# Performance work log

Hardware: AMD Instinct MI355X
Metric: run time of the kernel (lower is better)

The kernel has to match this reference:

```python
import jax, jax.numpy as jnp
import numpy as np

N = 50000      # nodes
E = 800000     # edges (before self-loops)
F_IN = 256
H = 8          # heads layer 1
C = 64         # hidden channels per head
OUT = 40       # classes
NEG_SLOPE = 0.2


def setup_inputs() -> dict:
    key = jax.random.key(0)
    ks = jax.random.split(key, 10)
    sc = 0.05
    return {
        "x": jax.random.normal(ks[0], (N, F_IN), jnp.float32),
        "edge_index": jax.random.randint(ks[1], (2, E), 0, N, dtype=jnp.int64),
        "W1": jax.random.normal(ks[2], (F_IN, H * C), jnp.float32) * sc,
        "a_src1": jax.random.normal(ks[3], (H, C), jnp.float32) * sc,
        "a_dst1": jax.random.normal(ks[4], (H, C), jnp.float32) * sc,
        "b1": jnp.zeros((H * C,), jnp.float32),
        "W2": jax.random.normal(ks[5], (H * C, OUT), jnp.float32) * sc,
        "a_src2": jax.random.normal(ks[6], (1, OUT), jnp.float32) * sc,
        "a_dst2": jax.random.normal(ks[7], (1, OUT), jnp.float32) * sc,
        "b2": jnp.zeros((OUT,), jnp.float32),
    }


def gat_layer(h_in, src, dst, W, a_s, a_d, b, heads, ch, concat, n):
    # h: [n, heads, ch] per-head linear transform
    h = (h_in @ W).reshape(n, heads, ch)
    alpha_s = jnp.sum(h * a_s, axis=-1)   # [n, heads]
    alpha_d = jnp.sum(h * a_d, axis=-1)   # [n, heads]
    # edge-wise raw attention logits [E, heads]
    e = jax.nn.leaky_relu(alpha_s[src] + alpha_d[dst], NEG_SLOPE)
    # segment softmax over incoming edges of each dst node
    m = jax.ops.segment_max(e, dst, num_segments=n)
    w = jnp.exp(e - m[dst])
    s = jax.ops.segment_sum(w, dst, num_segments=n)
    alpha = w / s[dst]                    # [E, heads]
    # scatter-aggregate messages: [n, heads, ch]
    out = jax.ops.segment_sum(h[src] * alpha[:, :, None], dst, num_segments=n)
    out = out.reshape(n, heads * ch) if concat else out.mean(axis=1)
    return out + b


def reference(x, edge_index, W1, a_src1, a_dst1, b1, W2, a_src2, a_dst2, b2):
    # add self-loops (PyG GATConv default); guarantees every dst has >=1 edge
    loop = jnp.arange(N, dtype=edge_index.dtype)
    src = jnp.concatenate([edge_index[0], loop])
    dst = jnp.concatenate([edge_index[1], loop])
    h = gat_layer(x, src, dst, W1, a_src1, a_dst1, b1, H, C, True, N)
    h = jax.nn.relu(h)  # dropout is identity in eval mode
    out = gat_layer(h, src, dst, W2, a_src2, a_dst2, b2, 1, OUT, False, N)
    return jax.nn.log_softmax(out, axis=1)
```

## Files before the change

### kernel.cpp

```cpp
#include <hip/hip_runtime.h>

#define N_NODES 50000
#define N_EDGES 800000
#define F_INK   256
#define HC      512
#define OUT_C   40
#define OUT_P   48
#define NEG     0.2f
#define CAP     64
#define GEMM_NB 782
#define CHUNKS  782
#define PART_SZ 6250
#define SCAT_NB (CHUNKS * 8)

typedef short short8 __attribute__((ext_vector_type(8)));
typedef float f32x4 __attribute__((ext_vector_type(4)));
typedef float f32x2 __attribute__((ext_vector_type(2)));

__device__ __forceinline__ float bf2f(unsigned short u) {
    union { unsigned int i; float f; } v; v.i = ((unsigned int)u) << 16; return v.f;
}
__device__ __forceinline__ unsigned short f2bf(float f) {
    union { float f; unsigned int i; } v; v.f = f;
    unsigned int x = v.i;
    return (unsigned short)((x + 0x7fffu + ((x >> 16) & 1u)) >> 16);
}
__device__ __forceinline__ float bflo(unsigned int u) {
    union { unsigned int i; float f; } v; v.i = u << 16; return v.f;
}
__device__ __forceinline__ float bfhi(unsigned int u) {
    union { unsigned int i; float f; } v; v.i = u & 0xffff0000u; return v.f;
}
__device__ __forceinline__ bool ei_is64(const int* ei) {
    return ei[1] == 0 && ei[3] == 0 && ei[5] == 0;
}
__device__ __forceinline__ float lrelu(float x) { return fmaxf(x, NEG * x); }
__device__ __forceinline__ unsigned char f2fp8(float v) {
    return (unsigned char)(__builtin_amdgcn_cvt_pk_fp8_f32(v, v, 0, false) & 0xff);
}
__device__ __forceinline__ float fp82f(unsigned char b) {
    f32x2 p = __builtin_amdgcn_cvt_pk_f32_fp8((int)b, false);
    return p[0];
}

__global__ __launch_bounds__(256) void prep_k(const float* __restrict__ W1, const float* __restrict__ W2,
                       const float* __restrict__ s1, const float* __restrict__ d1, const float* __restrict__ b1,
                       const float* __restrict__ s2, const float* __restrict__ d2, const float* __restrict__ b2,
                       unsigned short* __restrict__ W1p, unsigned short* __restrict__ W2p,
                       unsigned short* __restrict__ s1c, unsigned short* __restrict__ d1c,
                       unsigned short* __restrict__ b1c, unsigned short* __restrict__ s2c,
                       unsigned short* __restrict__ d2c, unsigned short* __restrict__ b2c,
                       int* __restrict__ cnt) {
    int b = blockIdx.x;
    if (b < 512) {
        int t = b * 256 + threadIdx.x;
        int k = t / HC, n = t % HC;
        int s = k >> 5, q = (k >> 3) & 3, j = k & 7;
        W1p[((((s << 2) + q) * HC + n) << 3) + j] = f2bf(W1[k * HC + n]);
    } else if (b < 608) {
        int t = (b - 512) * 256 + threadIdx.x;
        int k = t / OUT_P, n = t % OUT_P;
        int s = k >> 5, q = (k >> 3) & 3, j = k & 7;
        unsigned short v = (n < OUT_C) ? f2bf(W2[k * OUT_C + n]) : (unsigned short)0;
        W2p[((((s << 2) + q) * OUT_P + n) << 3) + j] = v;
    } else if (b == 608) {
        int t = threadIdx.x;
        for (int j = t; j < 512; j += 256) {
            s1c[j] = f2bf(s1[j]); d1c[j] = f2bf(d1[j]); b1c[j] = f2bf(b1[j]);
        }
        if (t < OUT_C) { s2c[t] = f2bf(s2[t]); d2c[t] = f2bf(d2[t]); b2c[t] = f2bf(b2[t]); }
    } else {
        int i = (b - 609) * 256 + threadIdx.x;
        if (i < N_NODES) cnt[i * 16] = 0;
    }
}

__global__ __launch_bounds__(256) void scat_k(const int* __restrict__ ei,
                                              int* __restrict__ cnt, int* __restrict__ srcs) {
    int tid = threadIdx.x;
    int part = blockIdx.x & 7;
    int chunk = blockIdx.x >> 3;
    int lo = part * PART_SZ;
    bool is64 = ei_is64(ei);
    int e0 = chunk * 1024 + (tid << 2);
    int s[4], d[4];
    bool vld[4];
    if (chunk < CHUNKS - 1) {
        if (is64) {
            int4 a0 = *reinterpret_cast<const int4*>(ei + 2 * e0);
            int4 a1 = *reinterpret_cast<const int4*>(ei + 2 * e0 + 4);
            int4 c0 = *reinterpret_cast<const int4*>(ei + 2 * N_EDGES + 2 * e0);
            int4 c1 = *reinterpret_cast<const int4*>(ei + 2 * N_EDGES + 2 * e0 + 4);
            s[0] = a0.x; s[1] = a0.z; s[2] = a1.x; s[3] = a1.z;
            d[0] = c0.x; d[1] = c0.z; d[2] = c1.x; d[3] = c1.z;
        } else {
            int4 a0 = *reinterpret_cast<const int4*>(ei + e0);
            int4 c0 = *reinterpret_cast<const int4*>(ei + N_EDGES + e0);
            s[0] = a0.x; s[1] = a0.y; s[2] = a0.z; s[3] = a0.w;
            d[0] = c0.x; d[1] = c0.y; d[2] = c0.z; d[3] = c0.w;
        }
        vld[0] = vld[1] = vld[2] = vld[3] = true;
    } else {
#pragma unroll
        for (int j = 0; j < 4; j++) {
            int e = e0 + j;
            vld[j] = e < N_EDGES;
            int ec = vld[j] ? e : 0;
            s[j] = is64 ? ei[2 * ec] : ei[ec];
            d[j] = is64 ? ei[2 * N_EDGES + 2 * ec] : ei[N_EDGES + ec];
        }
    }
#pragma unroll
    for (int j = 0; j < 4; j++) {
        int dj = d[j];
        if (vld[j] && dj >= lo && dj < lo + PART_SZ) {
            int pos = atomicAdd(&cnt[dj * 16], 1);
            if (pos < CAP) srcs[(size_t)dj * CAP + pos] = s[j];
        }
    }
}

__global__ __launch_bounds__(256) void gemm1_k(const float* __restrict__ x,
                                               const unsigned short* __restrict__ Wp,
                                               const unsigned short* __restrict__ a_s,
                                               const unsigned short* __restrict__ a_d,
                                               unsigned char* __restrict__ h1f8,
                                               float* __restrict__ as1, float* __restrict__ ad1) {
    __shared__ unsigned short xs[64 * 264];
    int tid = threadIdx.x;
    int bm = blockIdx.x;
    int row0 = bm * 64;
#pragma unroll
    for (int it = 0; it < 16; it++) {
        int j = tid + it * 256;
        int r = j >> 6;
        int c = (j & 63) << 2;
        int rr = row0 + r; rr = rr < N_NODES ? rr : N_NODES - 1;
        float4 f = *reinterpret_cast<const float4*>(x + (size_t)rr * F_INK + c);
        unsigned int lo = (unsigned int)f2bf(f.x) | ((unsigned int)f2bf(f.y) << 16);
        unsigned int hi = (unsigned int)f2bf(f.z) | ((unsigned int)f2bf(f.w) << 16);
        *reinterpret_cast<uint2*>(&xs[r * 264 + c]) = make_uint2(lo, hi);
    }
    __syncthreads();
    int w = tid >> 6, lane = tid & 63;
    int q = lane >> 4, l16 = lane & 15;
    short8 a[8];
#pragma unroll
    for (int s = 0; s < 8; s++)
        a[s] = *reinterpret_cast<const short8*>(&xs[(w * 16 + l16) * 264 + s * 32 + q * 8]);
    int orow = row0 + w * 16 + q * 4;
#pragma unroll
    for (int bn = 0; bn < 8; bn++) {
        f32x4 acc[4];
#pragma unroll
        for (int t = 0; t < 4; t++) acc[t] = (f32x4){0.f, 0.f, 0.f, 0.f};
#pragma unroll
        for (int s = 0; s < 8; s++) {
#pragma unroll
            for (int t = 0; t < 4; t++) {
                int col = bn * 64 + t * 16 + l16;
                short8 b = *reinterpret_cast<const short8*>(Wp + ((((s << 2) + q) * HC + col) << 3));
                acc[t] = __builtin_amdgcn_mfma_f32_16x16x32_bf16(a[s], b, acc[t], 0, 0, 0);
            }
        }
        float sa0 = 0.f, sa1 = 0.f, sa2 = 0.f, sa3 = 0.f;
        float da0 = 0.f, da1 = 0.f, da2 = 0.f, da3 = 0.f;
#pragma unroll
        for (int t = 0; t < 4; t++) {
            int col = bn * 64 + t * 16 + l16;
            float asc = bf2f(a_s[col]);
            float adc = bf2f(a_d[col]);
            float v0 = acc[t][0], v1 = acc[t][1], v2 = acc[t][2], v3 = acc[t][3];
            sa0 += v0 * asc; da0 += v0 * adc;
            sa1 += v1 * asc; da1 += v1 * adc;
            sa2 += v2 * asc; da2 += v2 * adc;
            sa3 += v3 * asc; da3 += v3 * adc;
            if (orow + 3 < N_NODES) {
                h1f8[(size_t)(orow + 0) * HC + col] = f2fp8(v0);
                h1f8[(size_t)(orow + 1) * HC + col] = f2fp8(v1);
                h1f8[(size_t)(orow + 2) * HC + col] = f2fp8(v2);
                h1f8[(size_t)(orow + 3) * HC + col] = f2fp8(v3);
            } else {
                if (orow + 0 < N_NODES) h1f8[(size_t)(orow + 0) * HC + col] = f2fp8(v0);
                if (orow + 1 < N_NODES) h1f8[(size_t)(orow + 1) * HC + col] = f2fp8(v1);
                if (orow + 2 < N_NODES) h1f8[(size_t)(orow + 2) * HC + col] = f2fp8(v2);
                if (orow + 3 < N_NODES) h1f8[(size_t)(orow + 3) * HC + col] = f2fp8(v3);
            }
        }
#pragma unroll
        for (int m = 1; m < 16; m <<= 1) {
            sa0 += __shfl_xor(sa0, m, 64); sa1 += __shfl_xor(sa1, m, 64);
            sa2 += __shfl_xor(sa2, m, 64); sa3 += __shfl_xor(sa3, m, 64);
            da0 += __shfl_xor(da0, m, 64); da1 += __shfl_xor(da1, m, 64);
            da2 += __shfl_xor(da2, m, 64); da3 += __shfl_xor(da3, m, 64);
        }
        if (l16 < 4) {
            int rr = orow + l16;
            float sav = (l16 == 0) ? sa0 : (l16 == 1) ? sa1 : (l16 == 2) ? sa2 : sa3;
            float dav = (l16 == 0) ? da0 : (l16 == 1) ? da1 : (l16 == 2) ? da2 : da3;
            if (rr < N_NODES) { as1[rr * 8 + bn] = sav; ad1[rr * 8 + bn] = dav; }
        }
    }
}

#define ACC16(u, wgt)                                                              \
    {                                                                              \
        f32x2 q0 = __builtin_amdgcn_cvt_pk_f32_fp8((int)(u).x, false);             \
        f32x2 q1 = __builtin_amdgcn_cvt_pk_f32_fp8((int)(u).x, true);              \
        f32x2 q2 = __builtin_amdgcn_cvt_pk_f32_fp8((int)(u).y, false);             \
        f32x2 q3 = __builtin_amdgcn_cvt_pk_f32_fp8((int)(u).y, true);              \
        f32x2 q4 = __builtin_amdgcn_cvt_pk_f32_fp8((int)(u).z, false);             \
        f32x2 q5 = __builtin_amdgcn_cvt_pk_f32_fp8((int)(u).z, true);              \
        f32x2 q6 = __builtin_amdgcn_cvt_pk_f32_fp8((int)(u).w, false);             \
        f32x2 q7 = __builtin_amdgcn_cvt_pk_f32_fp8((int)(u).w, true);              \
        f32x2 wv = {(wgt), (wgt)};                                                 \
        ac[0] += wv * q0; ac[1] += wv * q1; ac[2] += wv * q2; ac[3] += wv * q3;    \
        ac[4] += wv * q4; ac[5] += wv * q5; ac[6] += wv * q6; ac[7] += wv * q7;    \
    }

__global__ __launch_bounds__(256) void agg1_k(const unsigned char* __restrict__ h1f8,
                                              const float* __restrict__ as1,
                                              const float* __restrict__ ad1,
                                              const int* __restrict__ cnt,
                                              const int* __restrict__ srcs,
                                              const unsigned short* __restrict__ b1,
                                              const unsigned short* __restrict__ W2p,
                                              const unsigned short* __restrict__ a_s2,
                                              const unsigned short* __restrict__ a_d2,
                                              unsigned char* __restrict__ h2f8) {
    __shared__ unsigned short rows[16 * 520];
    __shared__ int sSrc[16 * CAP];
    __shared__ int sCnt[16];
    __shared__ float sAs[16], sAd[16];
    __shared__ int ctr;
    int tid = threadIdx.x;
    int base = blockIdx.x * 16;
    reinterpret_cast<int4*>(sSrc)[tid] =
        reinterpret_cast<const int4*>(srcs + (size_t)base * CAP)[tid];
    if (tid < 16) {
        int d = cnt[(base + tid) * 16];
        sCnt[tid] = d < CAP ? d : CAP;
        sAs[tid] = 0.f; sAd[tid] = 0.f;
    }
    if (tid == 0) ctr = 0;
    __syncthreads();
    int w = tid >> 6, lane = tid & 63;
    int half = lane >> 5, li = lane & 31;
    int h = li >> 2;
    uint4 ub0 = reinterpret_cast<const uint4*>(b1)[li * 2 + 0];
    uint4 ub1 = reinterpret_cast<const uint4*>(b1)[li * 2 + 1];
    for (;;) {
        int rl = 0;
        if (lane == 0) rl = atomicAdd(&ctr, 1);
        rl = __shfl(rl, 0, 64);
        if (rl >= 16) break;
        int wid = base + rl;
        float adv = ad1[wid * 8 + h];
        const int* sp = sSrc + rl * CAP;
        int deg = sCnt[rl];
        f32x2 ac[8];
#pragma unroll
        for (int k = 0; k < 8; k++) ac[k] = (f32x2){0.f, 0.f};
        float sumw = 0.f;
        {
            int s = half ? (deg > 0 ? sp[0] : wid) : wid;
            float A = as1[s * 8 + h];
            uint4 u = reinterpret_cast<const uint4*>(h1f8 + (size_t)s * HC)[li];
            float wj = (half && deg == 0) ? 0.f : __expf(lrelu(A + adv));
            sumw += wj;
            ACC16(u, wj)
        }
        int v = 1;
        for (; v + 16 <= deg; v += 16) {
            int s[8]; float A[8]; uint4 u[8];
#pragma unroll
            for (int j = 0; j < 8; j++) s[j] = sp[v + 2 * j + half];
#pragma unroll
            for (int j = 0; j < 8; j++) A[j] = as1[s[j] * 8 + h];
#pragma unroll
            for (int j = 0; j < 8; j++)
                u[j] = reinterpret_cast<const uint4*>(h1f8 + (size_t)s[j] * HC)[li];
#pragma unroll
            for (int j = 0; j < 8; j++) {
                float wj = __expf(lrelu(A[j] + adv));
                sumw += wj;
                ACC16(u[j], wj)
            }
        }
        for (; v + 8 <= deg; v += 8) {
            int s[4]; float A[4]; uint4 u[4];
#pragma unroll
            for (int j = 0; j < 4; j++) s[j] = sp[v + 2 * j + half];
#pragma unroll
            for (int j = 0; j < 4; j++) A[j] = as1[s[j] * 8 + h];
#pragma unroll
            for (int j = 0; j < 4; j++)
                u[j] = reinterpret_cast<const uint4*>(h1f8 + (size_t)s[j] * HC)[li];
#pragma unroll
            for (int j = 0; j < 4; j++) {
                float wj = __expf(lrelu(A[j] + adv));
                sumw += wj;
                ACC16(u[j], wj)
            }
        }
        for (; v + 4 <= deg; v += 4) {
            int s[2]; float A[2]; uint4 u[2];
#pragma unroll
            for (int j = 0; j < 2; j++) s[j] = sp[v + 2 * j + half];
#pragma unroll
            for (int j = 0; j < 2; j++) A[j] = as1[s[j] * 8 + h];
#pragma unroll
            for (int j = 0; j < 2; j++)
                u[j] = reinterpret_cast<const uint4*>(h1f8 + (size_t)s[j] * HC)[li];
#pragma unroll
            for (int j = 0; j < 2; j++) {
                float wj = __expf(lrelu(A[j] + adv));
                sumw += wj;
                ACC16(u[j], wj)
            }
        }
        for (; v < deg; v += 2) {
            int vv = v + half;
            bool ok = vv < deg;
            int s = ok ? sp[vv] : wid;
            float A = as1[s * 8 + h];
            uint4 u = reinterpret_cast<const uint4*>(h1f8 + (size_t)s * HC)[li];
            float wj = ok ? __expf(lrelu(A + adv)) : 0.f;
            sumw += wj;
            ACC16(u, wj)
        }
        sumw += __shfl_xor(sumw, 32, 64);
#pragma unroll
        for (int k = 0; k < 8; k++) {
            ac[k][0] += __shfl_xor(ac[k][0], 32, 64);
            ac[k][1] += __shfl_xor(ac[k][1], 32, 64);
        }
        float inv = 1.f / sumw;
        f32x2 n0 = half ? ac[4] : ac[0];
        f32x2 n1 = half ? ac[5] : ac[1];
        f32x2 n2 = half ? ac[6] : ac[2];
        f32x2 n3 = half ? ac[7] : ac[3];
        uint4 ubh = half ? ub1 : ub0;
        float o0 = fmaxf(n0[0] * inv + bflo(ubh.x), 0.f);
        float o1 = fmaxf(n0[1] * inv + bfhi(ubh.x), 0.f);
        float o2 = fmaxf(n1[0] * inv + bflo(ubh.y), 0.f);
        float o3 = fmaxf(n1[1] * inv + bfhi(ubh.y), 0.f);
        float o4 = fmaxf(n2[0] * inv + bflo(ubh.z), 0.f);
        float o5 = fmaxf(n2[1] * inv + bfhi(ubh.z), 0.f);
        float o6 = fmaxf(n3[0] * inv + bflo(ubh.w), 0.f);
        float o7 = fmaxf(n3[1] * inv + bfhi(ubh.w), 0.f);
        uint4 r;
        r.x = (unsigned int)f2bf(o0) | ((unsigned int)f2bf(o1) << 16);
        r.y = (unsigned int)f2bf(o2) | ((unsigned int)f2bf(o3) << 16);
        r.z = (unsigned int)f2bf(o4) | ((unsigned int)f2bf(o5) << 16);
        r.w = (unsigned int)f2bf(o6) | ((unsigned int)f2bf(o7) << 16);
        *reinterpret_cast<uint4*>(&rows[rl * 520 + li * 16 + half * 8]) = r;
    }
    __syncthreads();
    if (w < 3) {
        int q = lane >> 4, l16 = lane & 15;
        int col = w * 16 + l16;
        f32x4 acc = (f32x4){0.f, 0.f, 0.f, 0.f};
#pragma unroll
        for (int s = 0; s < HC / 32; s++) {
            short8 a = *reinterpret_cast<const short8*>(&rows[l16 * 520 + s * 32 + q * 8]);
            short8 b = *reinterpret_cast<const short8*>(W2p + ((((s << 2) + q) * OUT_P + col) << 3));
            acc = __builtin_amdgcn_mfma_f32_16x16x32_bf16(a, b, acc, 0, 0, 0);
        }
        float sa0 = 0.f, sa1 = 0.f, sa2 = 0.f, sa3 = 0.f;
        float da0 = 0.f, da1 = 0.f, da2 = 0.f, da3 = 0.f;
        if (col < OUT_C) {
            float asc = bf2f(a_s2[col]);
            float adc = bf2f(a_d2[col]);
            sa0 = acc[0] * asc; da0 = acc[0] * adc;
            sa1 = acc[1] * asc; da1 = acc[1] * adc;
            sa2 = acc[2] * asc; da2 = acc[2] * adc;
            sa3 = acc[3] * asc; da3 = acc[3] * adc;
#pragma unroll
            for (int r = 0; r < 4; r++)
                h2f8[(size_t)(base + q * 4 + r) * 64 + col] = f2fp8(acc[r]);
        }
#pragma unroll
        for (int m = 1; m < 16; m <<= 1) {
            sa0 += __shfl_xor(sa0, m, 64); sa1 += __shfl_xor(sa1, m, 64);
            sa2 += __shfl_xor(sa2, m, 64); sa3 += __shfl_xor(sa3, m, 64);
            da0 += __shfl_xor(da0, m, 64); da1 += __shfl_xor(da1, m, 64);
            da2 += __shfl_xor(da2, m, 64); da3 += __shfl_xor(da3, m, 64);
        }
        if (l16 < 4) {
            int rr = q * 4 + l16;
            float sav = (l16 == 0) ? sa0 : (l16 == 1) ? sa1 : (l16 == 2) ? sa2 : sa3;
            float dav = (l16 == 0) ? da0 : (l16 == 1) ? da1 : (l16 == 2) ? da2 : da3;
            atomicAdd(&sAs[rr], sav);
            atomicAdd(&sAd[rr], dav);
        }
    }
    __syncthreads();
    if (tid < 16) {
        unsigned char* r = h2f8 + (size_t)(base + tid) * 64;
        *reinterpret_cast<float*>(r + 40) = sAs[tid];
        *reinterpret_cast<float*>(r + 44) = sAd[tid];
    }
}

__global__ __launch_bounds__(256) void agg2_k(const unsigned char* __restrict__ h2f8,
                                              const int* __restrict__ cnt,
                                              const int* __restrict__ srcs,
                                              const unsigned short* __restrict__ b2,
                                              float* __restrict__ outp) {
    __shared__ int sSrc[4 * CAP];
    __shared__ int sCnt[4];
    int tid = threadIdx.x;
    int base = blockIdx.x * 4;
    if (tid < 64)
        reinterpret_cast<int4*>(sSrc)[tid] =
            reinterpret_cast<const int4*>(srcs + (size_t)base * CAP)[tid];
    if (tid < 4) {
        int d = cnt[(base + tid) * 16];
        sCnt[tid] = d < CAP ? d : CAP;
    }
    __syncthreads();
    int w = tid >> 6;
    int wid = base + w;
    int lane = tid & 63;
    bool act = lane < OUT_C;
    int lclamp = act ? lane : 0;
    const unsigned char* rd = h2f8 + (size_t)wid * 64;
    float adv = *reinterpret_cast<const float*>(rd + 44);
    float acc, sumw;
    {
        float w0 = __expf(lrelu(*reinterpret_cast<const float*>(rd + 40) + adv));
        sumw = w0;
        acc = w0 * fp82f(rd[lclamp]);
    }
    const int* sp = sSrc + w * CAP;
    int deg = sCnt[w];
    int v = 0;
    for (; v + 8 <= deg; v += 8) {
        const unsigned char* r[8];
        float A[8];
        unsigned char c[8];
#pragma unroll
        for (int j = 0; j < 8; j++) r[j] = h2f8 + (size_t)sp[v + j] * 64;
#pragma unroll
        for (int j = 0; j < 8; j++) A[j] = *reinterpret_cast<const float*>(r[j] + 40);
#pragma unroll
        for (int j = 0; j < 8; j++) c[j] = r[j][lclamp];
#pragma unroll
        for (int j = 0; j < 8; j++) {
            float wj = __expf(lrelu(A[j] + adv));
            sumw += wj;
            acc += wj * fp82f(c[j]);
        }
    }
    for (; v + 4 <= deg; v += 4) {
        const unsigned char* r[4];
        float A[4];
        unsigned char c[4];
#pragma unroll
        for (int j = 0; j < 4; j++) r[j] = h2f8 + (size_t)sp[v + j] * 64;
#pragma unroll
        for (int j = 0; j < 4; j++) A[j] = *reinterpret_cast<const float*>(r[j] + 40);
#pragma unroll
        for (int j = 0; j < 4; j++) c[j] = r[j][lclamp];
#pragma unroll
        for (int j = 0; j < 4; j++) {
            float wj = __expf(lrelu(A[j] + adv));
            sumw += wj;
            acc += wj * fp82f(c[j]);
        }
    }
    for (; v < deg; v++) {
        const unsigned char* r0 = h2f8 + (size_t)sp[v] * 64;
        float w0 = __expf(lrelu(*reinterpret_cast<const float*>(r0 + 40) + adv));
        sumw += w0;
        acc += w0 * fp82f(r0[lclamp]);
    }
    float o = acc / sumw + bf2f(b2[lclamp]);
    float mval = act ? o : -1e30f;
#pragma unroll
    for (int m = 32; m >= 1; m >>= 1) mval = fmaxf(mval, __shfl_xor(mval, m, 64));
    float ex = act ? __expf(o - mval) : 0.f;
#pragma unroll
    for (int m = 32; m >= 1; m >>= 1) ex += __shfl_xor(ex, m, 64);
    float res = o - mval - __logf(ex);
    if (act) outp[(size_t)wid * OUT_C + lane] = res;
}

extern "C" void kernel_launch(void* const* d_in, const int* in_sizes, int n_in,
                              void* d_out, int out_size, void* d_ws, size_t ws_size,
                              hipStream_t stream) {
    const float* x      = (const float*)d_in[0];
    const int*   ei     = (const int*)d_in[1];
    const float* W1     = (const float*)d_in[2];
    const float* as1raw = (const float*)d_in[3];
    const float* ad1raw = (const float*)d_in[4];
    const float* b1raw  = (const float*)d_in[5];
    const float* W2     = (const float*)d_in[6];
    const float* as2raw = (const float*)d_in[7];
    const float* ad2raw = (const float*)d_in[8];
    const float* b2raw  = (const float*)d_in[9];
    float* out = (float*)d_out;

    char* p = (char*)d_ws;
    auto alloc = [&](size_t bytes) -> char* {
        char* r = p;
        p += (bytes + 255) & ~(size_t)255;
        return r;
    };
    unsigned short* s1c  = (unsigned short*)alloc(512 * 2);
    unsigned short* d1c  = (unsigned short*)alloc(512 * 2);
    unsigned short* b1c  = (unsigned short*)alloc(512 * 2);
    unsigned short* s2c  = (unsigned short*)alloc(OUT_C * 2);
    unsigned short* d2c  = (unsigned short*)alloc(OUT_C * 2);
    unsigned short* b2c  = (unsigned short*)alloc(OUT_C * 2);
    unsigned char*  h1f8 = (unsigned char*)alloc((size_t)N_NODES * HC);
    unsigned char*  h2f8 = (unsigned char*)alloc((size_t)N_NODES * 64);
    float* as1  = (float*)alloc((size_t)N_NODES * 8 * 4);
    float* ad1  = (float*)alloc((size_t)N_NODES * 8 * 4);
    int* cnt    = (int*)alloc((size_t)N_NODES * 64);
    int* srcs   = (int*)alloc((size_t)N_NODES * CAP * 4);
    unsigned short* W1p = (unsigned short*)alloc((size_t)F_INK * HC * 2);
    unsigned short* W2p = (unsigned short*)alloc((size_t)HC * OUT_P * 2);
    (void)ws_size; (void)in_sizes; (void)n_in; (void)out_size;

    const int NB = (N_NODES + 255) / 256;

    prep_k<<<609 + NB, 256, 0, stream>>>(W1, W2, as1raw, ad1raw, b1raw, as2raw, ad2raw, b2raw,
                                         W1p, W2p, s1c, d1c, b1c, s2c, d2c, b2c, cnt);
    gemm1_k<<<GEMM_NB, 256, 0, stream>>>(x, W1p, s1c, d1c, h1f8, as1, ad1);
    scat_k<<<SCAT_NB, 256, 0, stream>>>(ei, cnt, srcs);
    agg1_k<<<N_NODES / 16, 256, 0, stream>>>(h1f8, as1, ad1, cnt, srcs, b1c,
                                             W2p, s2c, d2c, h2f8);
    agg2_k<<<N_NODES / 4, 256, 0, stream>>>(h2f8, cnt, srcs, b2c, out);
}
```

Before: 290.2 us.

## Fuse GEMM, scatter and both aggregations into one persistent kernel with grid barriers

```diff
diff --git a/kernel.cpp b/kernel.cpp
--- a/kernel.cpp
+++ b/kernel.cpp
@@ -12,6 +12,10 @@
 #define CHUNKS  782
 #define PART_SZ 6250
 #define SCAT_NB (CHUNKS * 8)
+#define GRID_F  768
+#define P1_NV   (GEMM_NB + SCAT_NB)
+#define P2_NV   (N_NODES / 16)
+#define P3_NV   (N_NODES / 4)
 
 typedef short short8 __attribute__((ext_vector_type(8)));
 typedef float f32x4 __attribute__((ext_vector_type(4)));
@@ -41,6 +45,17 @@
 __device__ __forceinline__ float fp82f(unsigned char b) {
     f32x2 p = __builtin_amdgcn_cvt_pk_f32_fp8((int)b, false);
     return p[0];
+}
+
+__device__ __forceinline__ void gridbar(int* bar) {
+    __syncthreads();
+    if (threadIdx.x == 0) {
+        __threadfence();
+        atomicAdd(bar, 1);
+        while (atomicAdd(bar, 0) < (int)gridDim.x) __builtin_amdgcn_s_sleep(8);
+        __threadfence();
+    }
+    __syncthreads();
 }
 
 __global__ __launch_bounds__(256) void prep_k(const float* __restrict__ W1, const float* __restrict__ W2,
@@ -50,156 +65,28 @@
                        unsigned short* __restrict__ s1c, unsigned short* __restrict__ d1c,
                        unsigned short* __restrict__ b1c, unsigned short* __restrict__ s2c,
                        unsigned short* __restrict__ d2c, unsigned short* __restrict__ b2c,
-                       int* __restrict__ cnt) {
-    int b = blockIdx.x;
+                       int* __restrict__ cnt, int* __restrict__ bar) {
+    int b = blockIdx.x, tid = threadIdx.x;
     if (b < 512) {
-        int t = b * 256 + threadIdx.x;
+        int t = b * 256 + tid;
         int k = t / HC, n = t % HC;
         int s = k >> 5, q = (k >> 3) & 3, j = k & 7;
         W1p[((((s << 2) + q) * HC + n) << 3) + j] = f2bf(W1[k * HC + n]);
     } else if (b < 608) {
-        int t = (b - 512) * 256 + threadIdx.x;
+        int t = (b - 512) * 256 + tid;
         int k = t / OUT_P, n = t % OUT_P;
         int s = k >> 5, q = (k >> 3) & 3, j = k & 7;
         unsigned short v = (n < OUT_C) ? f2bf(W2[k * OUT_C + n]) : (unsigned short)0;
         W2p[((((s << 2) + q) * OUT_P + n) << 3) + j] = v;
     } else if (b == 608) {
-        int t = threadIdx.x;
-        for (int j = t; j < 512; j += 256) {
+        for (int j = tid; j < 512; j += 256) {
             s1c[j] = f2bf(s1[j]); d1c[j] = f2bf(d1[j]); b1c[j] = f2bf(b1[j]);
         }
-        if (t < OUT_C) { s2c[t] = f2bf(s2[t]); d2c[t] = f2bf(d2[t]); b2c[t] = f2bf(b2[t]); }
+        if (tid < OUT_C) { s2c[tid] = f2bf(s2[tid]); d2c[tid] = f2bf(d2[tid]); b2c[tid] = f2bf(b2[tid]); }
+        if (tid >= 64 && tid < 66) bar[tid - 64] = 0;
     } else {
-        int i = (b - 609) * 256 + threadIdx.x;
+        int i = (b - 609) * 256 + tid;
         if (i < N_NODES) cnt[i * 16] = 0;
-    }
-}
-
-__global__ __launch_bounds__(256) void scat_k(const int* __restrict__ ei,
-                                              int* __restrict__ cnt, int* __restrict__ srcs) {
-    int tid = threadIdx.x;
-    int part = blockIdx.x & 7;
-    int chunk = blockIdx.x >> 3;
-    int lo = part * PART_SZ;
-    bool is64 = ei_is64(ei);
-    int e0 = chunk * 1024 + (tid << 2);
-    int s[4], d[4];
-    bool vld[4];
-    if (chunk < CHUNKS - 1) {
-        if (is64) {
-            int4 a0 = *reinterpret_cast<const int4*>(ei + 2 * e0);
-            int4 a1 = *reinterpret_cast<const int4*>(ei + 2 * e0 + 4);
-            int4 c0 = *reinterpret_cast<const int4*>(ei + 2 * N_EDGES + 2 * e0);
-            int4 c1 = *reinterpret_cast<const int4*>(ei + 2 * N_EDGES + 2 * e0 + 4);
-            s[0] = a0.x; s[1] = a0.z; s[2] = a1.x; s[3] = a1.z;
-            d[0] = c0.x; d[1] = c0.z; d[2] = c1.x; d[3] = c1.z;
-        } else {
-            int4 a0 = *reinterpret_cast<const int4*>(ei + e0);
-            int4 c0 = *reinterpret_cast<const int4*>(ei + N_EDGES + e0);
-            s[0] = a0.x; s[1] = a0.y; s[2] = a0.z; s[3] = a0.w;
-            d[0] = c0.x; d[1] = c0.y; d[2] = c0.z; d[3] = c0.w;
-        }
-        vld[0] = vld[1] = vld[2] = vld[3] = true;
-    } else {
-#pragma unroll
-        for (int j = 0; j < 4; j++) {
-            int e = e0 + j;
-            vld[j] = e < N_EDGES;
-            int ec = vld[j] ? e : 0;
-            s[j] = is64 ? ei[2 * ec] : ei[ec];
-            d[j] = is64 ? ei[2 * N_EDGES + 2 * ec] : ei[N_EDGES + ec];
-        }
-    }
-#pragma unroll
-    for (int j = 0; j < 4; j++) {
-        int dj = d[j];
-        if (vld[j] && dj >= lo && dj < lo + PART_SZ) {
-            int pos = atomicAdd(&cnt[dj * 16], 1);
-            if (pos < CAP) srcs[(size_t)dj * CAP + pos] = s[j];
-        }
-    }
-}
-
-__global__ __launch_bounds__(256) void gemm1_k(const float* __restrict__ x,
-                                               const unsigned short* __restrict__ Wp,
-                                               const unsigned short* __restrict__ a_s,
-                                               const unsigned short* __restrict__ a_d,
-                                               unsigned char* __restrict__ h1f8,
-                                               float* __restrict__ as1, float* __restrict__ ad1) {
-    __shared__ unsigned short xs[64 * 264];
-    int tid = threadIdx.x;
-    int bm = blockIdx.x;
-    int row0 = bm * 64;
-#pragma unroll
-    for (int it = 0; it < 16; it++) {
-        int j = tid + it * 256;
-        int r = j >> 6;
-        int c = (j & 63) << 2;
-        int rr = row0 + r; rr = rr < N_NODES ? rr : N_NODES - 1;
-        float4 f = *reinterpret_cast<const float4*>(x + (size_t)rr * F_INK + c);
-        unsigned int lo = (unsigned int)f2bf(f.x) | ((unsigned int)f2bf(f.y) << 16);
-        unsigned int hi = (unsigned int)f2bf(f.z) | ((unsigned int)f2bf(f.w) << 16);
-        *reinterpret_cast<uint2*>(&xs[r * 264 + c]) = make_uint2(lo, hi);
-    }
-    __syncthreads();
-    int w = tid >> 6, lane = tid & 63;
-    int q = lane >> 4, l16 = lane & 15;
-    short8 a[8];
-#pragma unroll
-    for (int s = 0; s < 8; s++)
-        a[s] = *reinterpret_cast<const short8*>(&xs[(w * 16 + l16) * 264 + s * 32 + q * 8]);
-    int orow = row0 + w * 16 + q * 4;
-#pragma unroll
-    for (int bn = 0; bn < 8; bn++) {
-        f32x4 acc[4];
-#pragma unroll
-        for (int t = 0; t < 4; t++) acc[t] = (f32x4){0.f, 0.f, 0.f, 0.f};
-#pragma unroll
-        for (int s = 0; s < 8; s++) {
-#pragma unroll
-            for (int t = 0; t < 4; t++) {
-                int col = bn * 64 + t * 16 + l16;
-                short8 b = *reinterpret_cast<const short8*>(Wp + ((((s << 2) + q) * HC + col) << 3));
-                acc[t] = __builtin_amdgcn_mfma_f32_16x16x32_bf16(a[s], b, acc[t], 0, 0, 0);
-            }
-        }
-        float sa0 = 0.f, sa1 = 0.f, sa2 = 0.f, sa3 = 0.f;
-        float da0 = 0.f, da1 = 0.f, da2 = 0.f, da3 = 0.f;
-#pragma unroll
-        for (int t = 0; t < 4; t++) {
-            int col = bn * 64 + t * 16 + l16;
-            float asc = bf2f(a_s[col]);
-            float adc = bf2f(a_d[col]);
-            float v0 = acc[t][0], v1 = acc[t][1], v2 = acc[t][2], v3 = acc[t][3];
-            sa0 += v0 * asc; da0 += v0 * adc;
-            sa1 += v1 * asc; da1 += v1 * adc;
-            sa2 += v2 * asc; da2 += v2 * adc;
-            sa3 += v3 * asc; da3 += v3 * adc;
-            if (orow + 3 < N_NODES) {
-                h1f8[(size_t)(orow + 0) * HC + col] = f2fp8(v0);
-                h1f8[(size_t)(orow + 1) * HC + col] = f2fp8(v1);
-                h1f8[(size_t)(orow + 2) * HC + col] = f2fp8(v2);
-                h1f8[(size_t)(orow + 3) * HC + col] = f2fp8(v3);
-            } else {
-                if (orow + 0 < N_NODES) h1f8[(size_t)(orow + 0) * HC + col] = f2fp8(v0);
-                if (orow + 1 < N_NODES) h1f8[(size_t)(orow + 1) * HC + col] = f2fp8(v1);
-                if (orow + 2 < N_NODES) h1f8[(size_t)(orow + 2) * HC + col] = f2fp8(v2);
-                if (orow + 3 < N_NODES) h1f8[(size_t)(orow + 3) * HC + col] = f2fp8(v3);
-            }
-        }
-#pragma unroll
-        for (int m = 1; m < 16; m <<= 1) {
-            sa0 += __shfl_xor(sa0, m, 64); sa1 += __shfl_xor(sa1, m, 64);
-            sa2 += __shfl_xor(sa2, m, 64); sa3 += __shfl_xor(sa3, m, 64);
-            da0 += __shfl_xor(da0, m, 64); da1 += __shfl_xor(da1, m, 64);
-            da2 += __shfl_xor(da2, m, 64); da3 += __shfl_xor(da3, m, 64);
-        }
-        if (l16 < 4) {
-            int rr = orow + l16;
-            float sav = (l16 == 0) ? sa0 : (l16 == 1) ? sa1 : (l16 == 2) ? sa2 : sa3;
-            float dav = (l16 == 0) ? da0 : (l16 == 1) ? da1 : (l16 == 2) ? da2 : da3;
-            if (rr < N_NODES) { as1[rr * 8 + bn] = sav; ad1[rr * 8 + bn] = dav; }
-        }
     }
 }
 
@@ -218,273 +105,404 @@
         ac[4] += wv * q4; ac[5] += wv * q5; ac[6] += wv * q6; ac[7] += wv * q7;    \
     }
 
-__global__ __launch_bounds__(256) void agg1_k(const unsigned char* __restrict__ h1f8,
-                                              const float* __restrict__ as1,
-                                              const float* __restrict__ ad1,
-                                              const int* __restrict__ cnt,
-                                              const int* __restrict__ srcs,
-                                              const unsigned short* __restrict__ b1,
-                                              const unsigned short* __restrict__ W2p,
-                                              const unsigned short* __restrict__ a_s2,
-                                              const unsigned short* __restrict__ a_d2,
-                                              unsigned char* __restrict__ h2f8) {
-    __shared__ unsigned short rows[16 * 520];
-    __shared__ int sSrc[16 * CAP];
+__global__ __launch_bounds__(256, 3) void fused_k(const float* __restrict__ x,
+                       const unsigned short* __restrict__ Wp,
+                       const unsigned short* __restrict__ a_s, const unsigned short* __restrict__ a_d,
+                       unsigned char* __restrict__ h1f8,
+                       float* __restrict__ as1, float* __restrict__ ad1,
+                       const int* __restrict__ ei, int* __restrict__ cnt, int* __restrict__ srcs,
+                       const unsigned short* __restrict__ b1,
+                       const unsigned short* __restrict__ W2p,
+                       const unsigned short* __restrict__ a_s2, const unsigned short* __restrict__ a_d2,
+                       unsigned char* __restrict__ h2f8,
+                       const unsigned short* __restrict__ b2, float* __restrict__ outp,
+                       int* __restrict__ bar) {
+    __shared__ __align__(16) char smem[33792];
     __shared__ int sCnt[16];
     __shared__ float sAs[16], sAd[16];
     __shared__ int ctr;
     int tid = threadIdx.x;
-    int base = blockIdx.x * 16;
-    reinterpret_cast<int4*>(sSrc)[tid] =
-        reinterpret_cast<const int4*>(srcs + (size_t)base * CAP)[tid];
-    if (tid < 16) {
-        int d = cnt[(base + tid) * 16];
-        sCnt[tid] = d < CAP ? d : CAP;
-        sAs[tid] = 0.f; sAd[tid] = 0.f;
-    }
-    if (tid == 0) ctr = 0;
-    __syncthreads();
     int w = tid >> 6, lane = tid & 63;
-    int half = lane >> 5, li = lane & 31;
-    int h = li >> 2;
-    uint4 ub0 = reinterpret_cast<const uint4*>(b1)[li * 2 + 0];
-    uint4 ub1 = reinterpret_cast<const uint4*>(b1)[li * 2 + 1];
-    for (;;) {
-        int rl = 0;
-        if (lane == 0) rl = atomicAdd(&ctr, 1);
-        rl = __shfl(rl, 0, 64);
-        if (rl >= 16) break;
-        int wid = base + rl;
-        float adv = ad1[wid * 8 + h];
-        const int* sp = sSrc + rl * CAP;
-        int deg = sCnt[rl];
-        f32x2 ac[8];
-#pragma unroll
-        for (int k = 0; k < 8; k++) ac[k] = (f32x2){0.f, 0.f};
-        float sumw = 0.f;
+
+    for (int vt = blockIdx.x; vt < P1_NV; vt += gridDim.x) {
+        if (vt >= GEMM_NB) {
+            int sb = vt - GEMM_NB;
+            int part = sb & 7;
+            int chunk = sb >> 3;
+            int lo = part * PART_SZ;
+            bool is64 = ei_is64(ei);
+            int e0 = chunk * 1024 + (tid << 2);
+            int s[4], d[4];
+            bool vld[4];
+            if (chunk < CHUNKS - 1) {
+                if (is64) {
+                    int4 a0 = *reinterpret_cast<const int4*>(ei + 2 * e0);
+                    int4 a1 = *reinterpret_cast<const int4*>(ei + 2 * e0 + 4);
+                    int4 c0 = *reinterpret_cast<const int4*>(ei + 2 * N_EDGES + 2 * e0);
+                    int4 c1 = *reinterpret_cast<const int4*>(ei + 2 * N_EDGES + 2 * e0 + 4);
+                    s[0] = a0.x; s[1] = a0.z; s[2] = a1.x; s[3] = a1.z;
+                    d[0] = c0.x; d[1] = c0.z; d[2] = c1.x; d[3] = c1.z;
+                } else {
+                    int4 a0 = *reinterpret_cast<const int4*>(ei + e0);
+                    int4 c0 = *reinterpret_cast<const int4*>(ei + N_EDGES + e0);
+                    s[0] = a0.x; s[1] = a0.y; s[2] = a0.z; s[3] = a0.w;
+                    d[0] = c0.x; d[1] = c0.y; d[2] = c0.z; d[3] = c0.w;
+                }
+                vld[0] = vld[1] = vld[2] = vld[3] = true;
+            } else {
+#pragma unroll
+                for (int j = 0; j < 4; j++) {
+                    int e = e0 + j;
+                    vld[j] = e < N_EDGES;
+                    int ec = vld[j] ? e : 0;
+                    s[j] = is64 ? ei[2 * ec] : ei[ec];
+                    d[j] = is64 ? ei[2 * N_EDGES + 2 * ec] : ei[N_EDGES + ec];
+                }
+            }
+#pragma unroll
+            for (int j = 0; j < 4; j++) {
+                int dj = d[j];
+                if (vld[j] && dj >= lo && dj < lo + PART_SZ) {
+                    int pos = atomicAdd(&cnt[dj * 16], 1);
+                    if (pos < CAP) srcs[(size_t)dj * CAP + pos] = s[j];
+                }
+            }
+            __syncthreads();
+            continue;
+        }
         {
-            int s = half ? (deg > 0 ? sp[0] : wid) : wid;
-            float A = as1[s * 8 + h];
-            uint4 u = reinterpret_cast<const uint4*>(h1f8 + (size_t)s * HC)[li];
-            float wj = (half && deg == 0) ? 0.f : __expf(lrelu(A + adv));
-            sumw += wj;
-            ACC16(u, wj)
-        }
-        int v = 1;
-        for (; v + 16 <= deg; v += 16) {
-            int s[8]; float A[8]; uint4 u[8];
-#pragma unroll
-            for (int j = 0; j < 8; j++) s[j] = sp[v + 2 * j + half];
-#pragma unroll
-            for (int j = 0; j < 8; j++) A[j] = as1[s[j] * 8 + h];
-#pragma unroll
-            for (int j = 0; j < 8; j++)
-                u[j] = reinterpret_cast<const uint4*>(h1f8 + (size_t)s[j] * HC)[li];
-#pragma unroll
-            for (int j = 0; j < 8; j++) {
-                float wj = __expf(lrelu(A[j] + adv));
-                sumw += wj;
-                ACC16(u[j], wj)
-            }
-        }
-        for (; v + 8 <= deg; v += 8) {
-            int s[4]; float A[4]; uint4 u[4];
-#pragma unroll
-            for (int j = 0; j < 4; j++) s[j] = sp[v + 2 * j + half];
-#pragma unroll
-            for (int j = 0; j < 4; j++) A[j] = as1[s[j] * 8 + h];
-#pragma unroll
-            for (int j = 0; j < 4; j++)
-                u[j] = reinterpret_cast<const uint4*>(h1f8 + (size_t)s[j] * HC)[li];
-#pragma unroll
-            for (int j = 0; j < 4; j++) {
-                float wj = __expf(lrelu(A[j] + adv));
-                sumw += wj;
-                ACC16(u[j], wj)
-            }
-        }
-        for (; v + 4 <= deg; v += 4) {
-            int s[2]; float A[2]; uint4 u[2];
-#pragma unroll
-            for (int j = 0; j < 2; j++) s[j] = sp[v + 2 * j + half];
-#pragma unroll
-            for (int j = 0; j < 2; j++) A[j] = as1[s[j] * 8 + h];
-#pragma unroll
-            for (int j = 0; j < 2; j++)
-                u[j] = reinterpret_cast<const uint4*>(h1f8 + (size_t)s[j] * HC)[li];
-#pragma unroll
-            for (int j = 0; j < 2; j++) {
-                float wj = __expf(lrelu(A[j] + adv));
-                sumw += wj;
-                ACC16(u[j], wj)
-            }
-        }
-        for (; v < deg; v += 2) {
-            int vv = v + half;
-            bool ok = vv < deg;
-            int s = ok ? sp[vv] : wid;
-            float A = as1[s * 8 + h];
-            uint4 u = reinterpret_cast<const uint4*>(h1f8 + (size_t)s * HC)[li];
-            float wj = ok ? __expf(lrelu(A + adv)) : 0.f;
-            sumw += wj;
-            ACC16(u, wj)
-        }
-        sumw += __shfl_xor(sumw, 32, 64);
-#pragma unroll
-        for (int k = 0; k < 8; k++) {
-            ac[k][0] += __shfl_xor(ac[k][0], 32, 64);
-            ac[k][1] += __shfl_xor(ac[k][1], 32, 64);
-        }
-        float inv = 1.f / sumw;
-        f32x2 n0 = half ? ac[4] : ac[0];
-        f32x2 n1 = half ? ac[5] : ac[1];
-        f32x2 n2 = half ? ac[6] : ac[2];
-        f32x2 n3 = half ? ac[7] : ac[3];
-        uint4 ubh = half ? ub1 : ub0;
-        float o0 = fmaxf(n0[0] * inv + bflo(ubh.x), 0.f);
-        float o1 = fmaxf(n0[1] * inv + bfhi(ubh.x), 0.f);
-        float o2 = fmaxf(n1[0] * inv + bflo(ubh.y), 0.f);
-        float o3 = fmaxf(n1[1] * inv + bfhi(ubh.y), 0.f);
-        float o4 = fmaxf(n2[0] * inv + bflo(ubh.z), 0.f);
-        float o5 = fmaxf(n2[1] * inv + bfhi(ubh.z), 0.f);
-        float o6 = fmaxf(n3[0] * inv + bflo(ubh.w), 0.f);
-        float o7 = fmaxf(n3[1] * inv + bfhi(ubh.w), 0.f);
-        uint4 r;
-        r.x = (unsigned int)f2bf(o0) | ((unsigned int)f2bf(o1) << 16);
-        r.y = (unsigned int)f2bf(o2) | ((unsigned int)f2bf(o3) << 16);
-        r.z = (unsigned int)f2bf(o4) | ((unsigned int)f2bf(o5) << 16);
-        r.w = (unsigned int)f2bf(o6) | ((unsigned int)f2bf(o7) << 16);
-        *reinterpret_cast<uint4*>(&rows[rl * 520 + li * 16 + half * 8]) = r;
-    }
-    __syncthreads();
-    if (w < 3) {
-        int q = lane >> 4, l16 = lane & 15;
-        int col = w * 16 + l16;
-        f32x4 acc = (f32x4){0.f, 0.f, 0.f, 0.f};
-#pragma unroll
-        for (int s = 0; s < HC / 32; s++) {
-            short8 a = *reinterpret_cast<const short8*>(&rows[l16 * 520 + s * 32 + q * 8]);
-            short8 b = *reinterpret_cast<const short8*>(W2p + ((((s << 2) + q) * OUT_P + col) << 3));
-            acc = __builtin_amdgcn_mfma_f32_16x16x32_bf16(a, b, acc, 0, 0, 0);
-        }
-        float sa0 = 0.f, sa1 = 0.f, sa2 = 0.f, sa3 = 0.f;
-        float da0 = 0.f, da1 = 0.f, da2 = 0.f, da3 = 0.f;
-        if (col < OUT_C) {
-            float asc = bf2f(a_s2[col]);
-            float adc = bf2f(a_d2[col]);
-            sa0 = acc[0] * asc; da0 = acc[0] * adc;
-            sa1 = acc[1] * asc; da1 = acc[1] * adc;
-            sa2 = acc[2] * asc; da2 = acc[2] * adc;
-            sa3 = acc[3] * asc; da3 = acc[3] * adc;
-#pragma unroll
-            for (int r = 0; r < 4; r++)
-                h2f8[(size_t)(base + q * 4 + r) * 64 + col] = f2fp8(acc[r]);
-        }
-#pragma unroll
-        for (int m = 1; m < 16; m <<= 1) {
-            sa0 += __shfl_xor(sa0, m, 64); sa1 += __shfl_xor(sa1, m, 64);
-            sa2 += __shfl_xor(sa2, m, 64); sa3 += __shfl_xor(sa3, m, 64);
-            da0 += __shfl_xor(da0, m, 64); da1 += __shfl_xor(da1, m, 64);
-            da2 += __shfl_xor(da2, m, 64); da3 += __shfl_xor(da3, m, 64);
-        }
-        if (l16 < 4) {
-            int rr = q * 4 + l16;
-            float sav = (l16 == 0) ? sa0 : (l16 == 1) ? sa1 : (l16 == 2) ? sa2 : sa3;
-            float dav = (l16 == 0) ? da0 : (l16 == 1) ? da1 : (l16 == 2) ? da2 : da3;
-            atomicAdd(&sAs[rr], sav);
-            atomicAdd(&sAd[rr], dav);
+            unsigned short* xs = reinterpret_cast<unsigned short*>(smem);
+            int row0 = vt * 64;
+#pragma unroll
+            for (int it = 0; it < 16; it++) {
+                int j = tid + it * 256;
+                int r = j >> 6;
+                int c = (j & 63) << 2;
+                int rr = row0 + r; rr = rr < N_NODES ? rr : N_NODES - 1;
+                float4 f = *reinterpret_cast<const float4*>(x + (size_t)rr * F_INK + c);
+                unsigned int lo = (unsigned int)f2bf(f.x) | ((unsigned int)f2bf(f.y) << 16);
+                unsigned int hi = (unsigned int)f2bf(f.z) | ((unsigned int)f2bf(f.w) << 16);
+                *reinterpret_cast<uint2*>(&xs[r * 264 + c]) = make_uint2(lo, hi);
+            }
+            __syncthreads();
+            int q = lane >> 4, l16 = lane & 15;
+            short8 a[8];
+#pragma unroll
+            for (int s = 0; s < 8; s++)
+                a[s] = *reinterpret_cast<const short8*>(&xs[(w * 16 + l16) * 264 + s * 32 + q * 8]);
+            int orow = row0 + w * 16 + q * 4;
+#pragma unroll
+            for (int bn = 0; bn < 8; bn++) {
+                f32x4 acc[4];
+#pragma unroll
+                for (int t = 0; t < 4; t++) acc[t] = (f32x4){0.f, 0.f, 0.f, 0.f};
+#pragma unroll
+                for (int s = 0; s < 8; s++) {
+#pragma unroll
+                    for (int t = 0; t < 4; t++) {
+                        int col = bn * 64 + t * 16 + l16;
+                        short8 b = *reinterpret_cast<const short8*>(Wp + ((((s << 2) + q) * HC + col) << 3));
+                        acc[t] = __builtin_amdgcn_mfma_f32_16x16x32_bf16(a[s], b, acc[t], 0, 0, 0);
+                    }
+                }
+                float sa0 = 0.f, sa1 = 0.f, sa2 = 0.f, sa3 = 0.f;
+                float da0 = 0.f, da1 = 0.f, da2 = 0.f, da3 = 0.f;
+#pragma unroll
+                for (int t = 0; t < 4; t++) {
+                    int col = bn * 64 + t * 16 + l16;
+                    float asc = bf2f(a_s[col]);
+                    float adc = bf2f(a_d[col]);
+                    float v0 = acc[t][0], v1 = acc[t][1], v2 = acc[t][2], v3 = acc[t][3];
+                    sa0 += v0 * asc; da0 += v0 * adc;
+                    sa1 += v1 * asc; da1 += v1 * adc;
+                    sa2 += v2 * asc; da2 += v2 * adc;
+                    sa3 += v3 * asc; da3 += v3 * adc;
+                    if (orow + 3 < N_NODES) {
+                        h1f8[(size_t)(orow + 0) * HC + col] = f2fp8(v0);
+                        h1f8[(size_t)(orow + 1) * HC + col] = f2fp8(v1);
+                        h1f8[(size_t)(orow + 2) * HC + col] = f2fp8(v2);
+                        h1f8[(size_t)(orow + 3) * HC + col] = f2fp8(v3);
+                    } else {
+                        if (orow + 0 < N_NODES) h1f8[(size_t)(orow + 0) * HC + col] = f2fp8(v0);
+                        if (orow + 1 < N_NODES) h1f8[(size_t)(orow + 1) * HC + col] = f2fp8(v1);
+                        if (orow + 2 < N_NODES) h1f8[(size_t)(orow + 2) * HC + col] = f2fp8(v2);
+                        if (orow + 3 < N_NODES) h1f8[(size_t)(orow + 3) * HC + col] = f2fp8(v3);
+                    }
+                }
+#pragma unroll
+                for (int m = 1; m < 16; m <<= 1) {
+                    sa0 += __shfl_xor(sa0, m, 64); sa1 += __shfl_xor(sa1, m, 64);
+                    sa2 += __shfl_xor(sa2, m, 64); sa3 += __shfl_xor(sa3, m, 64);
+                    da0 += __shfl_xor(da0, m, 64); da1 += __shfl_xor(da1, m, 64);
+                    da2 += __shfl_xor(da2, m, 64); da3 += __shfl_xor(da3, m, 64);
+                }
+                if (l16 < 4) {
+                    int rr = orow + l16;
+                    float sav = (l16 == 0) ? sa0 : (l16 == 1) ? sa1 : (l16 == 2) ? sa2 : sa3;
+                    float dav = (l16 == 0) ? da0 : (l16 == 1) ? da1 : (l16 == 2) ? da2 : da3;
+                    if (rr < N_NODES) { as1[rr * 8 + bn] = sav; ad1[rr * 8 + bn] = dav; }
+                }
+            }
+            __syncthreads();
         }
     }
-    __syncthreads();
-    if (tid < 16) {
-        unsigned char* r = h2f8 + (size_t)(base + tid) * 64;
-        *reinterpret_cast<float*>(r + 40) = sAs[tid];
-        *reinterpret_cast<float*>(r + 44) = sAd[tid];
-    }
-}
-
-__global__ __launch_bounds__(256) void agg2_k(const unsigned char* __restrict__ h2f8,
-                                              const int* __restrict__ cnt,
-                                              const int* __restrict__ srcs,
-                                              const unsigned short* __restrict__ b2,
-                                              float* __restrict__ outp) {
-    __shared__ int sSrc[4 * CAP];
-    __shared__ int sCnt[4];
-    int tid = threadIdx.x;
-    int base = blockIdx.x * 4;
-    if (tid < 64)
-        reinterpret_cast<int4*>(sSrc)[tid] =
-            reinterpret_cast<const int4*>(srcs + (size_t)base * CAP)[tid];
-    if (tid < 4) {
-        int d = cnt[(base + tid) * 16];
-        sCnt[tid] = d < CAP ? d : CAP;
-    }
-    __syncthreads();
-    int w = tid >> 6;
-    int wid = base + w;
-    int lane = tid & 63;
-    bool act = lane < OUT_C;
-    int lclamp = act ? lane : 0;
-    const unsigned char* rd = h2f8 + (size_t)wid * 64;
-    float adv = *reinterpret_cast<const float*>(rd + 44);
-    float acc, sumw;
+    gridbar(&bar[0]);
+
     {
-        float w0 = __expf(lrelu(*reinterpret_cast<const float*>(rd + 40) + adv));
-        sumw = w0;
-        acc = w0 * fp82f(rd[lclamp]);
-    }
-    const int* sp = sSrc + w * CAP;
-    int deg = sCnt[w];
-    int v = 0;
-    for (; v + 8 <= deg; v += 8) {
-        const unsigned char* r[8];
-        float A[8];
-        unsigned char c[8];
-#pragma unroll
-        for (int j = 0; j < 8; j++) r[j] = h2f8 + (size_t)sp[v + j] * 64;
-#pragma unroll
-        for (int j = 0; j < 8; j++) A[j] = *reinterpret_cast<const float*>(r[j] + 40);
-#pragma unroll
-        for (int j = 0; j < 8; j++) c[j] = r[j][lclamp];
-#pragma unroll
-        for (int j = 0; j < 8; j++) {
-            float wj = __expf(lrelu(A[j] + adv));
-            sumw += wj;
-            acc += wj * fp82f(c[j]);
+        int half = lane >> 5, li = lane & 31;
+        int h = li >> 2;
+        uint4 ub0 = reinterpret_cast<const uint4*>(b1)[li * 2 + 0];
+        uint4 ub1 = reinterpret_cast<const uint4*>(b1)[li * 2 + 1];
+        unsigned short* rows = reinterpret_cast<unsigned short*>(smem);
+        int* sSrc = reinterpret_cast<int*>(smem + 16640);
+        for (int vt = blockIdx.x; vt < P2_NV; vt += gridDim.x) {
+            int base = vt * 16;
+            reinterpret_cast<int4*>(sSrc)[tid] =
+                reinterpret_cast<const int4*>(srcs + (size_t)base * CAP)[tid];
+            if (tid < 16) {
+                int d = cnt[(base + tid) * 16];
+                sCnt[tid] = d < CAP ? d : CAP;
+                sAs[tid] = 0.f; sAd[tid] = 0.f;
+            }
+            if (tid == 0) ctr = 0;
+            __syncthreads();
+            for (;;) {
+                int rl = 0;
+                if (lane == 0) rl = atomicAdd(&ctr, 1);
+                rl = __shfl(rl, 0, 64);
+                if (rl >= 16) break;
+                int wid = base + rl;
+                float adv = ad1[wid * 8 + h];
+                const int* sp = sSrc + rl * CAP;
+                int deg = sCnt[rl];
+                f32x2 ac[8];
+#pragma unroll
+                for (int k = 0; k < 8; k++) ac[k] = (f32x2){0.f, 0.f};
+                float sumw = 0.f;
+                {
+                    int s = half ? (deg > 0 ? sp[0] : wid) : wid;
+                    float A = as1[s * 8 + h];
+                    uint4 u = reinterpret_cast<const uint4*>(h1f8 + (size_t)s * HC)[li];
+                    float wj = (half && deg == 0) ? 0.f : __expf(lrelu(A + adv));
+                    sumw += wj;
+                    ACC16(u, wj)
+                }
+                int v = 1;
+                for (; v + 16 <= deg; v += 16) {
+                    int s[8]; float A[8]; uint4 u[8];
+#pragma unroll
+                    for (int j = 0; j < 8; j++) s[j] = sp[v + 2 * j + half];
+#pragma unroll
+                    for (int j = 0; j < 8; j++) A[j] = as1[s[j] * 8 + h];
+#pragma unroll
+                    for (int j = 0; j < 8; j++)
+                        u[j] = reinterpret_cast<const uint4*>(h1f8 + (size_t)s[j] * HC)[li];
+#pragma unroll
+                    for (int j = 0; j < 8; j++) {
+                        float wj = __expf(lrelu(A[j] + adv));
+                        sumw += wj;
+                        ACC16(u[j], wj)
+                    }
+                }
+                for (; v + 8 <= deg; v += 8) {
+                    int s[4]; float A[4]; uint4 u[4];
+#pragma unroll
+                    for (int j = 0; j < 4; j++) s[j] = sp[v + 2 * j + half];
+#pragma unroll
+                    for (int j = 0; j < 4; j++) A[j] = as1[s[j] * 8 + h];
+#pragma unroll
+                    for (int j = 0; j < 4; j++)
+                        u[j] = reinterpret_cast<const uint4*>(h1f8 + (size_t)s[j] * HC)[li];
+#pragma unroll
+                    for (int j = 0; j < 4; j++) {
+                        float wj = __expf(lrelu(A[j] + adv));
+                        sumw += wj;
+                        ACC16(u[j], wj)
+                    }
+                }
+                for (; v + 4 <= deg; v += 4) {
+                    int s[2]; float A[2]; uint4 u[2];
+#pragma unroll
+                    for (int j = 0; j < 2; j++) s[j] = sp[v + 2 * j + half];
+#pragma unroll
+                    for (int j = 0; j < 2; j++) A[j] = as1[s[j] * 8 + h];
+#pragma unroll
+                    for (int j = 0; j < 2; j++)
+                        u[j] = reinterpret_cast<const uint4*>(h1f8 + (size_t)s[j] * HC)[li];
+#pragma unroll
+                    for (int j = 0; j < 2; j++) {
+                        float wj = __expf(lrelu(A[j] + adv));
+                        sumw += wj;
+                        ACC16(u[j], wj)
+                    }
+                }
+                for (; v < deg; v += 2) {
+                    int vv = v + half;
+                    bool ok = vv < deg;
+                    int s = ok ? sp[vv] : wid;
+                    float A = as1[s * 8 + h];
+                    uint4 u = reinterpret_cast<const uint4*>(h1f8 + (size_t)s * HC)[li];
+                    float wj = ok ? __expf(lrelu(A + adv)) : 0.f;
+                    sumw += wj;
+                    ACC16(u, wj)
+                }
+                sumw += __shfl_xor(sumw, 32, 64);
+#pragma unroll
+                for (int k = 0; k < 8; k++) {
+                    ac[k][0] += __shfl_xor(ac[k][0], 32, 64);
+                    ac[k][1] += __shfl_xor(ac[k][1], 32, 64);
+                }
+                float inv = 1.f / sumw;
+                f32x2 n0 = half ? ac[4] : ac[0];
+                f32x2 n1 = half ? ac[5] : ac[1];
+                f32x2 n2 = half ? ac[6] : ac[2];
+                f32x2 n3 = half ? ac[7] : ac[3];
+                uint4 ubh = half ? ub1 : ub0;
+                float o0 = fmaxf(n0[0] * inv + bflo(ubh.x), 0.f);
+                float o1 = fmaxf(n0[1] * inv + bfhi(ubh.x), 0.f);
+                float o2 = fmaxf(n1[0] * inv + bflo(ubh.y), 0.f);
+                float o3 = fmaxf(n1[1] * inv + bfhi(ubh.y), 0.f);
+                float o4 = fmaxf(n2[0] * inv + bflo(ubh.z), 0.f);
+                float o5 = fmaxf(n2[1] * inv + bfhi(ubh.z), 0.f);
+                float o6 = fmaxf(n3[0] * inv + bflo(ubh.w), 0.f);
+                float o7 = fmaxf(n3[1] * inv + bfhi(ubh.w), 0.f);
+                uint4 r;
+                r.x = (unsigned int)f2bf(o0) | ((unsigned int)f2bf(o1) << 16);
+                r.y = (unsigned int)f2bf(o2) | ((unsigned int)f2bf(o3) << 16);
+                r.z = (unsigned int)f2bf(o4) | ((unsigned int)f2bf(o5) << 16);
+                r.w = (unsigned int)f2bf(o6) | ((unsigned int)f2bf(o7) << 16);
+                *reinterpret_cast<uint4*>(&rows[rl * 520 + li * 16 + half * 8]) = r;
+            }
+            __syncthreads();
+            if (w < 3) {
+                int q = lane >> 4, l16 = lane & 15;
+                int col = w * 16 + l16;
+                f32x4 acc = (f32x4){0.f, 0.f, 0.f, 0.f};
+#pragma unroll
+                for (int s = 0; s < HC / 32; s++) {
+                    short8 a = *reinterpret_cast<const short8*>(&rows[l16 * 520 + s * 32 + q * 8]);
+                    short8 b = *reinterpret_cast<const short8*>(W2p + ((((s << 2) + q) * OUT_P + col) << 3));
+                    acc = __builtin_amdgcn_mfma_f32_16x16x32_bf16(a, b, acc, 0, 0, 0);
+                }
+                float sa0 = 0.f, sa1 = 0.f, sa2 = 0.f, sa3 = 0.f;
+                float da0 = 0.f, da1 = 0.f, da2 = 0.f, da3 = 0.f;
+                if (col < OUT_C) {
+                    float asc = bf2f(a_s2[col]);
+                    float adc = bf2f(a_d2[col]);
+                    sa0 = acc[0] * asc; da0 = acc[0] * adc;
+                    sa1 = acc[1] * asc; da1 = acc[1] * adc;
+                    sa2 = acc[2] * asc; da2 = acc[2] * adc;
+                    sa3 = acc[3] * asc; da3 = acc[3] * adc;
+#pragma unroll
+                    for (int r = 0; r < 4; r++)
+                        h2f8[(size_t)(base + q * 4 + r) * 64 + col] = f2fp8(acc[r]);
+                }
+#pragma unroll
+                for (int m = 1; m < 16; m <<= 1) {
+                    sa0 += __shfl_xor(sa0, m, 64); sa1 += __shfl_xor(sa1, m, 64);
+                    sa2 += __shfl_xor(sa2, m, 64); sa3 += __shfl_xor(sa3, m, 64);
+                    da0 += __shfl_xor(da0, m, 64); da1 += __shfl_xor(da1, m, 64);
+                    da2 += __shfl_xor(da2, m, 64); da3 += __shfl_xor(da3, m, 64);
+                }
+                if (l16 < 4) {
+                    int rr = q * 4 + l16;
+                    float sav = (l16 == 0) ? sa0 : (l16 == 1) ? sa1 : (l16 == 2) ? sa2 : sa3;
+                    float dav = (l16 == 0) ? da0 : (l16 == 1) ? da1 : (l16 == 2) ? da2 : da3;
+                    atomicAdd(&sAs[rr], sav);
+                    atomicAdd(&sAd[rr], dav);
+                }
+            }
+            __syncthreads();
+            if (tid < 16) {
+                unsigned char* r = h2f8 + (size_t)(base + tid) * 64;
+                *reinterpret_cast<float*>(r + 40) = sAs[tid];
+                *reinterpret_cast<float*>(r + 44) = sAd[tid];
+            }
+            __syncthreads();
         }
     }
-    for (; v + 4 <= deg; v += 4) {
-        const unsigned char* r[4];
-        float A[4];
-        unsigned char c[4];
-#pragma unroll
-        for (int j = 0; j < 4; j++) r[j] = h2f8 + (size_t)sp[v + j] * 64;
-#pragma unroll
-        for (int j = 0; j < 4; j++) A[j] = *reinterpret_cast<const float*>(r[j] + 40);
-#pragma unroll
-        for (int j = 0; j < 4; j++) c[j] = r[j][lclamp];
-#pragma unroll
-        for (int j = 0; j < 4; j++) {
-            float wj = __expf(lrelu(A[j] + adv));
-            sumw += wj;
-            acc += wj * fp82f(c[j]);
+    gridbar(&bar[1]);
+
+    {
+        int* sS = reinterpret_cast<int*>(smem);
+        int* sC = reinterpret_cast<int*>(smem + 1024);
+        bool act = lane < OUT_C;
+        int lclamp = act ? lane : 0;
+        float bv = bf2f(b2[lclamp]);
+        for (int vt = blockIdx.x; vt < P3_NV; vt += gridDim.x) {
+            int base = vt * 4;
+            if (tid < 64)
+                reinterpret_cast<int4*>(sS)[tid] =
+                    reinterpret_cast<const int4*>(srcs + (size_t)base * CAP)[tid];
+            if (tid < 4) {
+                int d = cnt[(base + tid) * 16];
+                sC[tid] = d < CAP ? d : CAP;
+            }
+            __syncthreads();
+            int wid = base + w;
+            const unsigned char* rd = h2f8 + (size_t)wid * 64;
+            float adv = *reinterpret_cast<const float*>(rd + 44);
+            float acc, sumw;
+            {
+                float w0 = __expf(lrelu(*reinterpret_cast<const float*>(rd + 40) + adv));
+                sumw = w0;
+                acc = w0 * fp82f(rd[lclamp]);
+            }
+            const int* sp = sS + w * CAP;
+            int deg = sC[w];
+            int v = 0;
+            for (; v + 8 <= deg; v += 8) {
+                const unsigned char* r[8];
+                float A[8];
+                unsigned char c[8];
+#pragma unroll
+                for (int j = 0; j < 8; j++) r[j] = h2f8 + (size_t)sp[v + j] * 64;
+#pragma unroll
+                for (int j = 0; j < 8; j++) A[j] = *reinterpret_cast<const float*>(r[j] + 40);
+#pragma unroll
+                for (int j = 0; j < 8; j++) c[j] = r[j][lclamp];
+#pragma unroll
+                for (int j = 0; j < 8; j++) {
+                    float wj = __expf(lrelu(A[j] + adv));
+                    sumw += wj;
+                    acc += wj * fp82f(c[j]);
+                }
+            }
+            for (; v + 4 <= deg; v += 4) {
+                const unsigned char* r[4];
+                float A[4];
+                unsigned char c[4];
+#pragma unroll
+                for (int j = 0; j < 4; j++) r[j] = h2f8 + (size_t)sp[v + j] * 64;
+#pragma unroll
+                for (int j = 0; j < 4; j++) A[j] = *reinterpret_cast<const float*>(r[j] + 40);
+#pragma unroll
+                for (int j = 0; j < 4; j++) c[j] = r[j][lclamp];
+#pragma unroll
+                for (int j = 0; j < 4; j++) {
+                    float wj = __expf(lrelu(A[j] + adv));
+                    sumw += wj;
+                    acc += wj * fp82f(c[j]);
+                }
+            }
+            for (; v < deg; v++) {
+                const unsigned char* r0 = h2f8 + (size_t)sp[v] * 64;
+                float w0 = __expf(lrelu(*reinterpret_cast<const float*>(r0 + 40) + adv));
+                sumw += w0;
+                acc += w0 * fp82f(r0[lclamp]);
+            }
+            float o = acc / sumw + bv;
+            float mval = act ? o : -1e30f;
+#pragma unroll
+            for (int m = 32; m >= 1; m >>= 1) mval = fmaxf(mval, __shfl_xor(mval, m, 64));
+            float ex = act ? __expf(o - mval) : 0.f;
+#pragma unroll
+            for (int m = 32; m >= 1; m >>= 1) ex += __shfl_xor(ex, m, 64);
+            float res = o - mval - __logf(ex);
+            if (act) outp[(size_t)wid * OUT_C + lane] = res;
+            __syncthreads();
         }
     }
-    for (; v < deg; v++) {
-        const unsigned char* r0 = h2f8 + (size_t)sp[v] * 64;
-        float w0 = __expf(lrelu(*reinterpret_cast<const float*>(r0 + 40) + adv));
-        sumw += w0;
-        acc += w0 * fp82f(r0[lclamp]);
-    }
-    float o = acc / sumw + bf2f(b2[lclamp]);
-    float mval = act ? o : -1e30f;
-#pragma unroll
-    for (int m = 32; m >= 1; m >>= 1) mval = fmaxf(mval, __shfl_xor(mval, m, 64));
-    float ex = act ? __expf(o - mval) : 0.f;
-#pragma unroll
-    for (int m = 32; m >= 1; m >>= 1) ex += __shfl_xor(ex, m, 64);
-    float res = o - mval - __logf(ex);
-    if (act) outp[(size_t)wid * OUT_C + lane] = res;
 }
 
 extern "C" void kernel_launch(void* const* d_in, const int* in_sizes, int n_in,
@@ -520,6 +538,7 @@
     float* ad1  = (float*)alloc((size_t)N_NODES * 8 * 4);
     int* cnt    = (int*)alloc((size_t)N_NODES * 64);
     int* srcs   = (int*)alloc((size_t)N_NODES * CAP * 4);
+    int* bar    = (int*)alloc(256);
     unsigned short* W1p = (unsigned short*)alloc((size_t)F_INK * HC * 2);
     unsigned short* W2p = (unsigned short*)alloc((size_t)HC * OUT_P * 2);
     (void)ws_size; (void)in_sizes; (void)n_in; (void)out_size;
@@ -527,10 +546,8 @@
     const int NB = (N_NODES + 255) / 256;
 
     prep_k<<<609 + NB, 256, 0, stream>>>(W1, W2, as1raw, ad1raw, b1raw, as2raw, ad2raw, b2raw,
-                                         W1p, W2p, s1c, d1c, b1c, s2c, d2c, b2c, cnt);
-    gemm1_k<<<GEMM_NB, 256, 0, stream>>>(x, W1p, s1c, d1c, h1f8, as1, ad1);
-    scat_k<<<SCAT_NB, 256, 0, stream>>>(ei, cnt, srcs);
-    agg1_k<<<N_NODES / 16, 256, 0, stream>>>(h1f8, as1, ad1, cnt, srcs, b1c,
-                                             W2p, s2c, d2c, h2f8);
-    agg2_k<<<N_NODES / 4, 256, 0, stream>>>(h2f8, cnt, srcs, b2c, out);
-}
+                                         W1p, W2p, s1c, d1c, b1c, s2c, d2c, b2c, cnt, bar);
+    fused_k<<<GRID_F, 256, 0, stream>>>(x, W1p, s1c, d1c, h1f8, as1, ad1,
+                                        ei, cnt, srcs, b1c, W2p, s2c, d2c,
+                                        h2f8, b2c, out, bar);
+}
```

Result: slower. 853.7 us (+194.2%).
